# Performance work log

Hardware: AMD Instinct MI355X
Metric: run time of the kernel (lower is better)

## Reference

```python
import jax, jax.numpy as jnp
import numpy as np

B, T, S, D, K = 512, 49, 200, 512, 128


def setup_inputs() -> dict:
    key = jax.random.key(0)
    ks = jax.random.split(key, 8)
    return {
        "ifeature": jax.random.normal(ks[0], (B, T, D), dtype=jnp.float32),
        "tfeature_h": jax.random.normal(ks[1], (B, S, D), dtype=jnp.float32),
        "w_Dense_Vi_0": jax.random.normal(ks[2], (D, K), dtype=jnp.float32) * 0.05,
        "w_Dense_Vt_0": jax.random.normal(ks[3], (D, K), dtype=jnp.float32) * 0.05,
        "w_Dense_Pi_0": jax.random.normal(ks[4], (2 * K, 1), dtype=jnp.float32) * 0.05,
        "b_Dense_Pi_0": jnp.zeros((T,), dtype=jnp.float32),
        "w_Dense_Vi_1": jax.random.normal(ks[5], (D, K), dtype=jnp.float32) * 0.05,
        "w_Dense_Vt_1": jax.random.normal(ks[6], (D, K), dtype=jnp.float32) * 0.05,
        "w_Dense_Pi_1": jax.random.normal(ks[7], (2 * K, 1), dtype=jnp.float32) * 0.05,
        "b_Dense_Pi_1": jnp.zeros((S,), dtype=jnp.float32),
    }


def reference(ifeature, tfeature_h, w_Dense_Vi_0, w_Dense_Vt_0, w_Dense_Pi_0,
              b_Dense_Pi_0, w_Dense_Vi_1, w_Dense_Vt_1, w_Dense_Pi_1, b_Dense_Pi_1):
    # tfeature: mean-pooled text, [B, D]
    tfeature = jnp.mean(tfeature_h, axis=1)

    # --- attention over image regions (title_len) ---
    w_Vi_0 = jnp.einsum('btd,dk->btk', ifeature, w_Dense_Vi_0)          # [B,T,K]
    w_Vt_0 = (tfeature @ w_Dense_Vt_0)[:, None, :]                      # [B,1,K] broadcast to T
    Hi = jnp.tanh(jnp.concatenate(
        [w_Vi_0, jnp.broadcast_to(w_Vt_0, w_Vi_0.shape)], axis=-1))     # [B,T,2K]
    Hi_w_b = jnp.einsum('btk,k->bt', Hi, w_Dense_Pi_0[:, 0]) + b_Dense_Pi_0
    Pi = jax.nn.softmax(Hi_w_b, axis=-1)                                # [B,T]
    Vi = jnp.einsum('bt,btd->bd', Pi, ifeature)                         # attended image feature

    # --- attention over text tokens (seq_len) ---
    w_Vi_1 = (Vi @ w_Dense_Vi_1)[:, None, :]                            # [B,1,K]
    w_Vt_1 = jnp.einsum('bsd,dk->bsk', tfeature_h, w_Dense_Vt_1)        # [B,S,K]
    Ht = jnp.tanh(jnp.concatenate(
        [jnp.broadcast_to(w_Vi_1, w_Vt_1.shape), w_Vt_1], axis=-1))     # [B,S,2K]
    Ht_b = jnp.einsum('bsk,k->bs', Ht, w_Dense_Pi_1[:, 0]) + b_Dense_Pi_1
    Pt = jax.nn.softmax(Ht_b, axis=-1)                                  # [B,S]

    # NOTE: original call() returns Pt_Vt (weighted tokens), not the pooled Vt.
    Pt_Vt = Pt[:, :, None] * tfeature_h                                 # [B,S,D]
    return Pt_Vt
```

## Files before the change

### kernel.cpp

```cpp
#include <hip/hip_runtime.h>
#include <math.h>

#define BB 512
#define SS 200
#define DD 512
#define KK 128
#define RR (BB * SS)

typedef __attribute__((ext_vector_type(8))) short bf16x8;
typedef __attribute__((ext_vector_type(4))) float f32x4;

__device__ inline unsigned short f2bf(float f) {
    union { float f; unsigned int u; } v; v.f = f;
    unsigned int r = v.u + 0x7FFFu + ((v.u >> 16) & 1u);
    return (unsigned short)(r >> 16);
}

__device__ inline bf16x8 pack8(const float4& a, const float4& b) {
    bf16x8 p;
    p[0] = (short)f2bf(a.x); p[1] = (short)f2bf(a.y);
    p[2] = (short)f2bf(a.z); p[3] = (short)f2bf(a.w);
    p[4] = (short)f2bf(b.x); p[5] = (short)f2bf(b.y);
    p[6] = (short)f2bf(b.z); p[7] = (short)f2bf(b.w);
    return p;
}

__global__ void wt_kernel(const float* __restrict__ W, unsigned short* __restrict__ Wt2) {
    int i = blockIdx.x * 256 + threadIdx.x;
    int j = i & 7;
    int l = (i >> 3) & 63;
    int n = (i >> 9) & 7;
    int t = i >> 12;
    int k = n * 16 + (l & 15);
    int d = t * 32 + (l >> 4) * 8 + j;
    Wt2[i] = f2bf(W[d * KK + k]);
}

__global__ __launch_bounds__(256, 2) void logits_frag_kernel(
    const float* __restrict__ tfh,
    const unsigned short* __restrict__ Wt2,
    const float* __restrict__ wpk,
    const float* __restrict__ bias,
    float* __restrict__ logits)
{
    int tid = threadIdx.x;
    int w   = tid >> 6;
    int l   = tid & 63;
    int l15 = l & 15;
    int g   = l >> 4;
    int brow = blockIdx.x * 128;

    int row0 = brow + w * 32 + l15;
    const float* a0 = tfh + (size_t)row0 * DD + g * 8;
    const float* a1 = a0 + 16 * DD;
    const unsigned short* bp = Wt2 + (size_t)l * 8;

    f32x4 acc[2][8];
    #pragma unroll
    for (int m = 0; m < 2; ++m)
        #pragma unroll
        for (int n = 0; n < 8; ++n) acc[m][n] = (f32x4){0.f, 0.f, 0.f, 0.f};

    float4 cA00 = *(const float4*)(a0);
    float4 cA01 = *(const float4*)(a0 + 4);
    float4 cA10 = *(const float4*)(a1);
    float4 cA11 = *(const float4*)(a1 + 4);

    #pragma unroll 2
    for (int t = 0; t < 16; ++t) {
        float4 nA00, nA01, nA10, nA11;
        if (t < 15) {
            int d = (t + 1) * 32;
            nA00 = *(const float4*)(a0 + d);
            nA01 = *(const float4*)(a0 + d + 4);
            nA10 = *(const float4*)(a1 + d);
            nA11 = *(const float4*)(a1 + d + 4);
        }
        bf16x8 af0 = pack8(cA00, cA01);
        bf16x8 af1 = pack8(cA10, cA11);
        const unsigned short* bt = bp + (size_t)t * (8 * 64 * 8);
        {
            bf16x8 b0 = *(const bf16x8*)(bt);
            bf16x8 b1 = *(const bf16x8*)(bt + 1 * 512);
            bf16x8 b2 = *(const bf16x8*)(bt + 2 * 512);
            bf16x8 b3 = *(const bf16x8*)(bt + 3 * 512);
            acc[0][0] = __builtin_amdgcn_mfma_f32_16x16x32_bf16(af0, b0, acc[0][0], 0, 0, 0);
            acc[1][0] = __builtin_amdgcn_mfma_f32_16x16x32_bf16(af1, b0, acc[1][0], 0, 0, 0);
            acc[0][1] = __builtin_amdgcn_mfma_f32_16x16x32_bf16(af0, b1, acc[0][1], 0, 0, 0);
            acc[1][1] = __builtin_amdgcn_mfma_f32_16x16x32_bf16(af1, b1, acc[1][1], 0, 0, 0);
            acc[0][2] = __builtin_amdgcn_mfma_f32_16x16x32_bf16(af0, b2, acc[0][2], 0, 0, 0);
            acc[1][2] = __builtin_amdgcn_mfma_f32_16x16x32_bf16(af1, b2, acc[1][2], 0, 0, 0);
            acc[0][3] = __builtin_amdgcn_mfma_f32_16x16x32_bf16(af0, b3, acc[0][3], 0, 0, 0);
            acc[1][3] = __builtin_amdgcn_mfma_f32_16x16x32_bf16(af1, b3, acc[1][3], 0, 0, 0);
        }
        {
            bf16x8 b4 = *(const bf16x8*)(bt + 4 * 512);
            bf16x8 b5 = *(const bf16x8*)(bt + 5 * 512);
            bf16x8 b6 = *(const bf16x8*)(bt + 6 * 512);
            bf16x8 b7 = *(const bf16x8*)(bt + 7 * 512);
            acc[0][4] = __builtin_amdgcn_mfma_f32_16x16x32_bf16(af0, b4, acc[0][4], 0, 0, 0);
            acc[1][4] = __builtin_amdgcn_mfma_f32_16x16x32_bf16(af1, b4, acc[1][4], 0, 0, 0);
            acc[0][5] = __builtin_amdgcn_mfma_f32_16x16x32_bf16(af0, b5, acc[0][5], 0, 0, 0);
            acc[1][5] = __builtin_amdgcn_mfma_f32_16x16x32_bf16(af1, b5, acc[1][5], 0, 0, 0);
            acc[0][6] = __builtin_amdgcn_mfma_f32_16x16x32_bf16(af0, b6, acc[0][6], 0, 0, 0);
            acc[1][6] = __builtin_amdgcn_mfma_f32_16x16x32_bf16(af1, b6, acc[1][6], 0, 0, 0);
            acc[0][7] = __builtin_amdgcn_mfma_f32_16x16x32_bf16(af0, b7, acc[0][7], 0, 0, 0);
            acc[1][7] = __builtin_amdgcn_mfma_f32_16x16x32_bf16(af1, b7, acc[1][7], 0, 0, 0);
        }
        cA00 = nA00; cA01 = nA01; cA10 = nA10; cA11 = nA11;
    }

    float wv[8];
    #pragma unroll
    for (int n = 0; n < 8; ++n) wv[n] = wpk[n * 16 + l15];

    float rs[2][4];
    #pragma unroll
    for (int m = 0; m < 2; ++m)
        #pragma unroll
        for (int r = 0; r < 4; ++r) rs[m][r] = 0.f;
    #pragma unroll
    for (int m = 0; m < 2; ++m)
        #pragma unroll
        for (int n = 0; n < 8; ++n)
            #pragma unroll
            for (int r = 0; r < 4; ++r)
                rs[m][r] += tanhf(acc[m][n][r]) * wv[n];
    #pragma unroll
    for (int m = 0; m < 2; ++m)
        #pragma unroll
        for (int r = 0; r < 4; ++r) {
            float v = rs[m][r];
            v += __shfl_xor(v, 1, 64);
            v += __shfl_xor(v, 2, 64);
            v += __shfl_xor(v, 4, 64);
            v += __shfl_xor(v, 8, 64);
            rs[m][r] = v;
        }
    if (l15 == 0) {
        #pragma unroll
        for (int m = 0; m < 2; ++m)
            #pragma unroll
            for (int r = 0; r < 4; ++r) {
                int grow = brow + w * 32 + m * 16 + g * 4 + r;
                int s = grow % SS;
                logits[grow] = rs[m][r] + bias[s];
            }
    }
}

__global__ __launch_bounds__(1024) void softmax_mul_kernel(
    const float* __restrict__ logits,
    const float* __restrict__ tfh,
    float* __restrict__ out)
{
    int b = blockIdx.x;
    int tid = threadIdx.x;
    __shared__ float Pt[SS];
    __shared__ float wpart[16];

    float v = (tid < SS) ? logits[(size_t)b * SS + tid] : -INFINITY;
    float m = v;
    #pragma unroll
    for (int off = 32; off > 0; off >>= 1) m = fmaxf(m, __shfl_xor(m, off, 64));
    if ((tid & 63) == 0) wpart[tid >> 6] = m;
    __syncthreads();
    m = -INFINITY;
    #pragma unroll
    for (int i = 0; i < 16; ++i) m = fmaxf(m, wpart[i]);
    float e = (tid < SS) ? expf(v - m) : 0.f;
    float ssum = e;
    #pragma unroll
    for (int off = 32; off > 0; off >>= 1) ssum += __shfl_xor(ssum, off, 64);
    __syncthreads();
    if ((tid & 63) == 0) wpart[tid >> 6] = ssum;
    __syncthreads();
    ssum = 0.f;
    #pragma unroll
    for (int i = 0; i < 16; ++i) ssum += wpart[i];
    if (tid < SS) Pt[tid] = e / ssum;
    __syncthreads();

    const f32x4* src = (const f32x4*)(tfh + (size_t)b * SS * DD);
    f32x4*       dst = (f32x4*)(out + (size_t)b * SS * DD);
    const int n4 = SS * DD / 4;
    for (int i = tid; i < n4; i += 1024) {
        float p = Pt[i >> 7];
        f32x4 x = src[i];
        x = x * p;
        __builtin_nontemporal_store(x, dst + i);
    }
}

extern "C" void kernel_launch(void* const* d_in, const int* in_sizes, int n_in,
                              void* d_out, int out_size, void* d_ws, size_t ws_size,
                              hipStream_t stream) {
    const float* tfh   = (const float*)d_in[1];
    const float* wVt1  = (const float*)d_in[7];
    const float* wp1   = (const float*)d_in[8];
    const float* bias1 = (const float*)d_in[9];
    float* out = (float*)d_out;

    unsigned short* Wt2 = (unsigned short*)d_ws;
    float* logits = (float*)((char*)d_ws + 16 * 8 * 64 * 8 * sizeof(unsigned short));

    wt_kernel<<<(16 * 8 * 64 * 8) / 256, 256, 0, stream>>>(wVt1, Wt2);
    logits_frag_kernel<<<RR / 128, 256, 0, stream>>>(tfh, Wt2, wp1 + KK, bias1, logits);
    softmax_mul_kernel<<<BB, 1024, 0, stream>>>(logits, tfh, out);
}
```

Measured before the change: 140.1 us.

## Stage A tiles through LDS with coalesced loads and use fast tanh

Threads now load A in a coalesced row-major pattern, convert it to bf16 and write it into a shared-memory tile, then read MFMA fragments from LDS. This replaces the strided per-lane global loads and register prefetching. Occupancy is raised to 4 blocks/CU, and tanhf is replaced with an exp2/rcp approximation. The cost is two barriers per k-step and the loss of explicit prefetch overlap, with a slight accuracy change in tanh.

```diff
diff --git a/kernel.cpp b/kernel.cpp
--- a/kernel.cpp
+++ b/kernel.cpp
@@ -8,6 +8,7 @@
 #define RR (BB * SS)
 
 typedef __attribute__((ext_vector_type(8))) short bf16x8;
+typedef __attribute__((ext_vector_type(4))) short bf16x4;
 typedef __attribute__((ext_vector_type(4))) float f32x4;
 
 __device__ inline unsigned short f2bf(float f) {
@@ -16,13 +17,10 @@
     return (unsigned short)(r >> 16);
 }
 
-__device__ inline bf16x8 pack8(const float4& a, const float4& b) {
-    bf16x8 p;
-    p[0] = (short)f2bf(a.x); p[1] = (short)f2bf(a.y);
-    p[2] = (short)f2bf(a.z); p[3] = (short)f2bf(a.w);
-    p[4] = (short)f2bf(b.x); p[5] = (short)f2bf(b.y);
-    p[6] = (short)f2bf(b.z); p[7] = (short)f2bf(b.w);
-    return p;
+__device__ inline float fast_tanh(float x) {
+    x = fminf(10.f, fmaxf(-10.f, x));
+    float t = exp2f(x * 2.885390081777927f);
+    return (t - 1.f) * __builtin_amdgcn_rcpf(t + 1.f);
 }
 
 __global__ void wt_kernel(const float* __restrict__ W, unsigned short* __restrict__ Wt2) {
@@ -36,13 +34,15 @@
     Wt2[i] = f2bf(W[d * KK + k]);
 }
 
-__global__ __launch_bounds__(256, 2) void logits_frag_kernel(
+__global__ __launch_bounds__(256, 4) void logits_kernel(
     const float* __restrict__ tfh,
     const unsigned short* __restrict__ Wt2,
     const float* __restrict__ wpk,
     const float* __restrict__ bias,
     float* __restrict__ logits)
 {
+    __shared__ unsigned short As[128][40];
+
     int tid = threadIdx.x;
     int w   = tid >> 6;
     int l   = tid & 63;
@@ -50,9 +50,10 @@
     int g   = l >> 4;
     int brow = blockIdx.x * 128;
 
-    int row0 = brow + w * 32 + l15;
-    const float* a0 = tfh + (size_t)row0 * DD + g * 8;
-    const float* a1 = a0 + 16 * DD;
+    int r0 = tid >> 3;
+    int c4 = tid & 7;
+    const float* ap = tfh + (size_t)(brow + r0) * DD + c4 * 4;
+
     const unsigned short* bp = Wt2 + (size_t)l * 8;
 
     f32x4 acc[2][8];
@@ -61,53 +62,30 @@
         #pragma unroll
         for (int n = 0; n < 8; ++n) acc[m][n] = (f32x4){0.f, 0.f, 0.f, 0.f};
 
-    float4 cA00 = *(const float4*)(a0);
-    float4 cA01 = *(const float4*)(a0 + 4);
-    float4 cA10 = *(const float4*)(a1);
-    float4 cA11 = *(const float4*)(a1 + 4);
-
-    #pragma unroll 2
     for (int t = 0; t < 16; ++t) {
-        float4 nA00, nA01, nA10, nA11;
-        if (t < 15) {
-            int d = (t + 1) * 32;
-            nA00 = *(const float4*)(a0 + d);
-            nA01 = *(const float4*)(a0 + d + 4);
-            nA10 = *(const float4*)(a1 + d);
-            nA11 = *(const float4*)(a1 + d + 4);
+        int d0 = t * 32;
+        #pragma unroll
+        for (int jj = 0; jj < 4; ++jj) {
+            float4 v = *(const float4*)(ap + d0 + (size_t)(32 * jj) * DD);
+            bf16x4 p;
+            p[0] = (short)f2bf(v.x); p[1] = (short)f2bf(v.y);
+            p[2] = (short)f2bf(v.z); p[3] = (short)f2bf(v.w);
+            *(bf16x4*)&As[r0 + 32 * jj][c4 * 4] = p;
         }
-        bf16x8 af0 = pack8(cA00, cA01);
-        bf16x8 af1 = pack8(cA10, cA11);
+        __syncthreads();
+        bf16x8 af0 = *(const bf16x8*)&As[w * 32 + l15][g * 8];
+        bf16x8 af1 = *(const bf16x8*)&As[w * 32 + 16 + l15][g * 8];
         const unsigned short* bt = bp + (size_t)t * (8 * 64 * 8);
-        {
-            bf16x8 b0 = *(const bf16x8*)(bt);
-            bf16x8 b1 = *(const bf16x8*)(bt + 1 * 512);
-            bf16x8 b2 = *(const bf16x8*)(bt + 2 * 512);
-            bf16x8 b3 = *(const bf16x8*)(bt + 3 * 512);
-            acc[0][0] = __builtin_amdgcn_mfma_f32_16x16x32_bf16(af0, b0, acc[0][0], 0, 0, 0);
-            acc[1][0] = __builtin_amdgcn_mfma_f32_16x16x32_bf16(af1, b0, acc[1][0], 0, 0, 0);
-            acc[0][1] = __builtin_amdgcn_mfma_f32_16x16x32_bf16(af0, b1, acc[0][1], 0, 0, 0);
-            acc[1][1] = __builtin_amdgcn_mfma_f32_16x16x32_bf16(af1, b1, acc[1][1], 0, 0, 0);
-            acc[0][2] = __builtin_amdgcn_mfma_f32_16x16x32_bf16(af0, b2, acc[0][2], 0, 0, 0);
-            acc[1][2] = __builtin_amdgcn_mfma_f32_16x16x32_bf16(af1, b2, acc[1][2], 0, 0, 0);
-            acc[0][3] = __builtin_amdgcn_mfma_f32_16x16x32_bf16(af0, b3, acc[0][3], 0, 0, 0);
-            acc[1][3] = __builtin_amdgcn_mfma_f32_16x16x32_bf16(af1, b3, acc[1][3], 0, 0, 0);
+        #pragma unroll
+        for (int nb = 0; nb < 4; ++nb) {
+            bf16x8 b0 = *(const bf16x8*)(bt + (2 * nb) * 512);
+            bf16x8 b1 = *(const bf16x8*)(bt + (2 * nb + 1) * 512);
+            acc[0][2*nb]   = __builtin_amdgcn_mfma_f32_16x16x32_bf16(af0, b0, acc[0][2*nb],   0, 0, 0);
+            acc[1][2*nb]   = __builtin_amdgcn_mfma_f32_16x16x32_bf16(af1, b0, acc[1][2*nb],   0, 0, 0);
+            acc[0][2*nb+1] = __builtin_amdgcn_mfma_f32_16x16x32_bf16(af0, b1, acc[0][2*nb+1], 0, 0, 0);
+            acc[1][2*nb+1] = __builtin_amdgcn_mfma_f32_16x16x32_bf16(af1, b1, acc[1][2*nb+1], 0, 0, 0);
         }
-        {
-            bf16x8 b4 = *(const bf16x8*)(bt + 4 * 512);
-            bf16x8 b5 = *(const bf16x8*)(bt + 5 * 512);
-            bf16x8 b6 = *(const bf16x8*)(bt + 6 * 512);
-            bf16x8 b7 = *(const bf16x8*)(bt + 7 * 512);
-            acc[0][4] = __builtin_amdgcn_mfma_f32_16x16x32_bf16(af0, b4, acc[0][4], 0, 0, 0);
-            acc[1][4] = __builtin_amdgcn_mfma_f32_16x16x32_bf16(af1, b4, acc[1][4], 0, 0, 0);
-            acc[0][5] = __builtin_amdgcn_mfma_f32_16x16x32_bf16(af0, b5, acc[0][5], 0, 0, 0);
-            acc[1][5] = __builtin_amdgcn_mfma_f32_16x16x32_bf16(af1, b5, acc[1][5], 0, 0, 0);
-            acc[0][6] = __builtin_amdgcn_mfma_f32_16x16x32_bf16(af0, b6, acc[0][6], 0, 0, 0);
-            acc[1][6] = __builtin_amdgcn_mfma_f32_16x16x32_bf16(af1, b6, acc[1][6], 0, 0, 0);
-            acc[0][7] = __builtin_amdgcn_mfma_f32_16x16x32_bf16(af0, b7, acc[0][7], 0, 0, 0);
-            acc[1][7] = __builtin_amdgcn_mfma_f32_16x16x32_bf16(af1, b7, acc[1][7], 0, 0, 0);
-        }
-        cA00 = nA00; cA01 = nA01; cA10 = nA10; cA11 = nA11;
+        __syncthreads();
     }
 
     float wv[8];
@@ -125,7 +103,7 @@
         for (int n = 0; n < 8; ++n)
             #pragma unroll
             for (int r = 0; r < 4; ++r)
-                rs[m][r] += tanhf(acc[m][n][r]) * wv[n];
+                rs[m][r] += fast_tanh(acc[m][n][r]) * wv[n];
     #pragma unroll
     for (int m = 0; m < 2; ++m)
         #pragma unroll
@@ -143,8 +121,7 @@
             #pragma unroll
             for (int r = 0; r < 4; ++r) {
                 int grow = brow + w * 32 + m * 16 + g * 4 + r;
-                int s = grow % SS;
-                logits[grow] = rs[m][r] + bias[s];
+                logits[grow] = rs[m][r] + bias[grow % SS];
             }
     }
 }
@@ -205,6 +182,6 @@
     float* logits = (float*)((char*)d_ws + 16 * 8 * 64 * 8 * sizeof(unsigned short));
 
     wt_kernel<<<(16 * 8 * 64 * 8) / 256, 256, 0, stream>>>(wVt1, Wt2);
-    logits_frag_kernel<<<RR / 128, 256, 0, stream>>>(tfh, Wt2, wp1 + KK, bias1, logits);
+    logits_kernel<<<RR / 128, 256, 0, stream>>>(tfh, Wt2, wp1 + KK, bias1, logits);
     softmax_mul_kernel<<<BB, 1024, 0, stream>>>(logits, tfh, out);
 }
```

Measured after the change: 116.5 us. -16.8%, faster.
